# Kernel tuning notes

Measured on AMD Instinct MI355X. Metric: run time of the kernel, lower is better.

The kernel has to match this reference:

```python
import jax, jax.numpy as jnp
import numpy as np

TEMPERATURE = 8.0

def _non_neg(x):
    # exp(x) for x<0, x+1 for x>=0 (non-negative feature map)
    return jnp.where(x < 0, jnp.exp(x), x + 1.0)

def setup_inputs() -> dict:
    key = jax.random.key(0)
    kq, kk, kv, km = jax.random.split(key, 4)
    B, H, S, D = 8, 16, 4096, 64
    q = jax.random.normal(kq, (B, H, S, D), dtype=jnp.float32)
    k = jax.random.normal(kk, (B, H, S, D), dtype=jnp.float32)
    v = jax.random.normal(kv, (B, H, S, D), dtype=jnp.float32)
    token_mask = jax.random.randint(km, (B, S), 0, 2).astype(bool)
    return {"q": q, "k": k, "v": v, "token_mask": token_mask}

def reference(q, k, v, token_mask):
    B, H, S, D = q.shape
    idx = jnp.arange(S, dtype=q.dtype)
    cos_vec = jnp.cos(jnp.pi / 2.0 / S * idx)[:, None]  # [S,1], broadcasts over D
    sin_vec = jnp.sin(jnp.pi / 2.0 / S * idx)[:, None]
    qf = _non_neg(q)
    kf = _non_neg(k)
    q_cos = qf * cos_vec
    q_sin = qf * sin_vec
    k_cos = kf * cos_vec
    k_sin = kf * sin_vec
    mask = token_mask[:, None, :, None].astype(q.dtype)  # [B,1,S,1]
    q_cos = q_cos * mask
    q_sin = q_sin * mask
    # global context: [B,H,D,Dv]
    k_cos_v = jnp.einsum('bhsd,bhse->bhde', k_cos, v)
    k_sin_v = jnp.einsum('bhsd,bhse->bhde', k_sin, v)
    values = (jnp.einsum('bhsd,bhde->bhse', q_cos, k_cos_v)
              + jnp.einsum('bhsd,bhde->bhse', q_sin, k_sin_v)) / TEMPERATURE
    return values
```

## Files before the change

### kernel.cpp

```cpp
#include <hip/hip_runtime.h>
#include <math.h>

#define Sn 4096
#define Dn 64
#define CW 3.834951969714103e-4f
#define P1S 34

typedef __attribute__((ext_vector_type(8))) short short8;
typedef __attribute__((ext_vector_type(4))) float f32x4;

__device__ __forceinline__ unsigned short f2bf(float x) {
    unsigned int u = __float_as_uint(x);
    u += 0x7fffu + ((u >> 16) & 1u);
    return (unsigned short)(u >> 16);
}
__device__ __forceinline__ unsigned int pack2(float lo, float hi) {
    return (unsigned int)f2bf(lo) | ((unsigned int)f2bf(hi) << 16);
}
__device__ __forceinline__ float nneg(float x) {
    return x < 0.f ? __expf(x) : x + 1.f;
}
__device__ __forceinline__ short8 ld_frag(const unsigned int* p) {
    uint2 a = *(const uint2*)p;
    uint2 b = *(const uint2*)(p + 2);
    union { unsigned int u[4]; short8 s; } r;
    r.u[0] = a.x; r.u[1] = a.y; r.u[2] = b.x; r.u[3] = b.y;
    return r.s;
}

__global__ __launch_bounds__(256) void k_init(float4* kv4, int* flag,
                                              const unsigned char* mask_raw) {
    int i = blockIdx.x * 256 + threadIdx.x;
    kv4[i] = make_float4(0.f, 0.f, 0.f, 0.f);
    if (blockIdx.x == 0) {
        __shared__ int s_any;
        if (threadIdx.x == 0) s_any = 0;
        __syncthreads();
        int any = 0;
        int base = threadIdx.x * 16;
        #pragma unroll
        for (int j = 0; j < 16; j++) {
            int idx = base + j;
            if ((idx & 3) && mask_raw[idx]) any = 1;
        }
        if (any) s_any = 1;
        __syncthreads();
        if (threadIdx.x == 0) *flag = s_any ? 0 : 1;
    }
}

__global__ __launch_bounds__(256) void k_phase1(const float* __restrict__ kk,
                                                const float* __restrict__ vv,
                                                float* __restrict__ kv) {
    __shared__ unsigned int ldsKc[64 * P1S];
    __shared__ unsigned int ldsKs[64 * P1S];
    __shared__ unsigned int ldsV [64 * P1S];
    const int t    = threadIdx.x;
    const int bh   = blockIdx.x >> 4;
    const int sblk = (blockIdx.x & 15) << 8;
    const int c    = t & 15;
    const int rp   = t >> 4;
    const int lane = t & 63;
    const int w    = t >> 6;
    const int n    = lane & 15;
    const int q4   = lane >> 4;
    const float* kb = kk + (size_t)bh * (Sn * Dn);
    const float* vb = vv + (size_t)bh * (Sn * Dn);

    f32x4 accC[4], accS[4];
    #pragma unroll
    for (int i = 0; i < 4; i++) {
        accC[i] = (f32x4){0.f, 0.f, 0.f, 0.f};
        accS[i] = (f32x4){0.f, 0.f, 0.f, 0.f};
    }

    float4 pk[2][4], pv[2][4];
    {
        const float* kp = kb + (size_t)(sblk + rp * 4) * Dn + c * 4;
        const float* vp = vb + (size_t)(sblk + rp * 4) * Dn + c * 4;
        #pragma unroll
        for (int i = 0; i < 4; i++) {
            pk[0][i] = *(const float4*)(kp + i * Dn);
            pv[0][i] = *(const float4*)(vp + i * Dn);
        }
    }

    #pragma unroll
    for (int chunk = 0; chunk < 4; chunk++) {
        const int cur = chunk & 1, nxt = cur ^ 1;
        const int s0 = sblk + chunk * 64;
        float cs[4], sn[4], fk[4][4], fv[4][4];
        #pragma unroll
        for (int i = 0; i < 4; i++) {
            __sincosf(CW * (float)(s0 + rp * 4 + i), &sn[i], &cs[i]);
            fk[i][0] = nneg(pk[cur][i].x); fk[i][1] = nneg(pk[cur][i].y);
            fk[i][2] = nneg(pk[cur][i].z); fk[i][3] = nneg(pk[cur][i].w);
            fv[i][0] = pv[cur][i].x; fv[i][1] = pv[cur][i].y;
            fv[i][2] = pv[cur][i].z; fv[i][3] = pv[cur][i].w;
        }
        #pragma unroll
        for (int j = 0; j < 4; j++) {
            int d = c * 4 + j;
            uint2 wc, wsn, wv;
            wc.x  = pack2(fk[0][j] * cs[0], fk[1][j] * cs[1]);
            wc.y  = pack2(fk[2][j] * cs[2], fk[3][j] * cs[3]);
            wsn.x = pack2(fk[0][j] * sn[0], fk[1][j] * sn[1]);
            wsn.y = pack2(fk[2][j] * sn[2], fk[3][j] * sn[3]);
            wv.x  = pack2(fv[0][j], fv[1][j]);
            wv.y  = pack2(fv[2][j], fv[3][j]);
            *(uint2*)&ldsKc[d * P1S + rp * 2] = wc;
            *(uint2*)&ldsKs[d * P1S + rp * 2] = wsn;
            *(uint2*)&ldsV [d * P1S + rp * 2] = wv;
        }
        __syncthreads();
        if (chunk < 3) {
            const float* kp = kb + (size_t)(s0 + 64 + rp * 4) * Dn + c * 4;
            const float* vp = vb + (size_t)(s0 + 64 + rp * 4) * Dn + c * 4;
            #pragma unroll
            for (int i = 0; i < 4; i++) {
                pk[nxt][i] = *(const float4*)(kp + i * Dn);
                pv[nxt][i] = *(const float4*)(vp + i * Dn);
            }
        }
        #pragma unroll
        for (int ks = 0; ks < 2; ks++) {
            short8 Bv = ld_frag(&ldsV[(w * 16 + n) * P1S + ks * 16 + q4 * 4]);
            #pragma unroll
            for (int dt = 0; dt < 4; dt++) {
                short8 Ac = ld_frag(&ldsKc[(dt * 16 + n) * P1S + ks * 16 + q4 * 4]);
                short8 As = ld_frag(&ldsKs[(dt * 16 + n) * P1S + ks * 16 + q4 * 4]);
                accC[dt] = __builtin_amdgcn_mfma_f32_16x16x32_bf16(Ac, Bv, accC[dt], 0, 0, 0);
                accS[dt] = __builtin_amdgcn_mfma_f32_16x16x32_bf16(As, Bv, accS[dt], 0, 0, 0);
            }
        }
        __syncthreads();
    }
    float* base = kv + (size_t)bh * 2 * 4096;
    const int e = w * 16 + n;
    #pragma unroll
    for (int dt = 0; dt < 4; dt++) {
        #pragma unroll
        for (int r = 0; r < 4; r++) {
            int d = dt * 16 + q4 * 4 + r;
            atomicAdd(base +        d * 64 + e, accC[dt][r]);
            atomicAdd(base + 4096 + d * 64 + e, accS[dt][r]);
        }
    }
}

__global__ __launch_bounds__(256) void k_phase2(const float* __restrict__ qq,
                                                const void* __restrict__ mask_raw,
                                                const float* __restrict__ kv,
                                                const int* __restrict__ flag,
                                                float* __restrict__ out) {
    const int t    = threadIdx.x;
    const int bh   = blockIdx.x >> 4;
    const int sblk = (blockIdx.x & 15) << 8;
    const int b    = bh >> 4;
    const int lane = t & 63;
    const int w    = t >> 6;
    const int n    = lane & 15;
    const int q4   = lane >> 4;
    const int iflag = *flag;

    const float* kvb = kv + (size_t)bh * 8192;
    short8 Bc[4][2], Bs[4][2];
    #pragma unroll
    for (int et = 0; et < 4; et++) {
        const int e = et * 16 + n;
        #pragma unroll
        for (int ks = 0; ks < 2; ks++) {
            const int d0 = ks * 32 + q4 * 8;
            union { unsigned int u[4]; short8 s; } uc, us;
            #pragma unroll
            for (int jj = 0; jj < 4; jj++) {
                float c0 = kvb[(size_t)(d0 + 2 * jj)     * 64 + e];
                float c1 = kvb[(size_t)(d0 + 2 * jj + 1) * 64 + e];
                float s0 = kvb[4096 + (size_t)(d0 + 2 * jj)     * 64 + e];
                float s1 = kvb[4096 + (size_t)(d0 + 2 * jj + 1) * 64 + e];
                uc.u[jj] = pack2(c0, c1);
                us.u[jj] = pack2(s0, s1);
            }
            Bc[et][ks] = uc.s;
            Bs[et][ks] = us.s;
        }
    }

    const float* qb = qq + (size_t)bh * (Sn * Dn);
    float* ob       = out + (size_t)bh * (Sn * Dn);
    const unsigned char* m8 = (const unsigned char*)mask_raw;
    const int* m32          = (const int*)mask_raw;

    float4 pq[2][4];
    float  pmv[2];
    {
        int s_row = sblk + w * 16 + n;
        const float* qp = qb + (size_t)s_row * Dn + q4 * 8;
        pq[0][0] = *(const float4*)(qp);
        pq[0][1] = *(const float4*)(qp + 4);
        pq[0][2] = *(const float4*)(qp + 32);
        pq[0][3] = *(const float4*)(qp + 36);
        pmv[0] = iflag ? (m32[b * Sn + s_row] ? 1.f : 0.f)
                       : (m8 [b * Sn + s_row] ? 1.f : 0.f);
    }

    #pragma unroll
    for (int strip = 0; strip < 4; strip++) {
        const int cur = strip & 1, nxt = cur ^ 1;
        const int s_base = sblk + strip * 64 + w * 16;
        const int s_row  = s_base + n;
        float cs, snv;
        __sincosf(CW * (float)s_row, &snv, &cs);
        cs *= pmv[cur]; snv *= pmv[cur];
        float f[16];
        f[0]  = nneg(pq[cur][0].x); f[1]  = nneg(pq[cur][0].y);
        f[2]  = nneg(pq[cur][0].z); f[3]  = nneg(pq[cur][0].w);
        f[4]  = nneg(pq[cur][1].x); f[5]  = nneg(pq[cur][1].y);
        f[6]  = nneg(pq[cur][1].z); f[7]  = nneg(pq[cur][1].w);
        f[8]  = nneg(pq[cur][2].x); f[9]  = nneg(pq[cur][2].y);
        f[10] = nneg(pq[cur][2].z); f[11] = nneg(pq[cur][2].w);
        f[12] = nneg(pq[cur][3].x); f[13] = nneg(pq[cur][3].y);
        f[14] = nneg(pq[cur][3].z); f[15] = nneg(pq[cur][3].w);
        short8 Ac0, As0, Ac1, As1;
        #pragma unroll
        for (int j = 0; j < 8; j++) {
            Ac0[j] = (short)f2bf(f[j] * cs);
            As0[j] = (short)f2bf(f[j] * snv);
            Ac1[j] = (short)f2bf(f[8 + j] * cs);
            As1[j] = (short)f2bf(f[8 + j] * snv);
        }
        if (strip < 3) {
            int s_row2 = sblk + (strip + 1) * 64 + w * 16 + n;
            const float* qp = qb + (size_t)s_row2 * Dn + q4 * 8;
            pq[nxt][0] = *(const float4*)(qp);
            pq[nxt][1] = *(const float4*)(qp + 4);
            pq[nxt][2] = *(const float4*)(qp + 32);
            pq[nxt][3] = *(const float4*)(qp + 36);
            pmv[nxt] = iflag ? (m32[b * Sn + s_row2] ? 1.f : 0.f)
                             : (m8 [b * Sn + s_row2] ? 1.f : 0.f);
        }
        f32x4 acc[4];
        #pragma unroll
        for (int et = 0; et < 4; et++) acc[et] = (f32x4){0.f, 0.f, 0.f, 0.f};
        #pragma unroll
        for (int et = 0; et < 4; et++) {
            acc[et] = __builtin_amdgcn_mfma_f32_16x16x32_bf16(Ac0, Bc[et][0], acc[et], 0, 0, 0);
            acc[et] = __builtin_amdgcn_mfma_f32_16x16x32_bf16(Ac1, Bc[et][1], acc[et], 0, 0, 0);
            acc[et] = __builtin_amdgcn_mfma_f32_16x16x32_bf16(As0, Bs[et][0], acc[et], 0, 0, 0);
            acc[et] = __builtin_amdgcn_mfma_f32_16x16x32_bf16(As1, Bs[et][1], acc[et], 0, 0, 0);
        }
        #pragma unroll
        for (int et = 0; et < 4; et++) {
            #pragma unroll
            for (int r = 0; r < 4; r++) {
                int row = q4 * 4 + r;
                ob[(size_t)(s_base + row) * 64 + et * 16 + n] = acc[et][r] * 0.125f;
            }
        }
    }
}

extern "C" void kernel_launch(void* const* d_in, const int* in_sizes, int n_in,
                              void* d_out, int out_size, void* d_ws, size_t ws_size,
                              hipStream_t stream) {
    const float* q = (const float*)d_in[0];
    const float* k = (const float*)d_in[1];
    const float* v = (const float*)d_in[2];
    const void* mask = d_in[3];
    int*   flag = (int*)d_ws;
    float* kv   = (float*)((char*)d_ws + 256);

    k_init  <<<1024, 256, 0, stream>>>((float4*)kv, flag, (const unsigned char*)mask);
    k_phase1<<<2048, 256, 0, stream>>>(k, v, kv);
    k_phase2<<<2048, 256, 0, stream>>>(q, mask, kv, flag, (float*)d_out);
}
```

Measured before the change: 424.4 us.

## Double-buffer phase1 LDS, halve its grid, and use cheaper bf16 packing

Phase1 now double-buffers its LDS tiles, which removes the trailing barrier in each chunk. Each block also processes 512 sequence rows instead of 256, halving the grid and the number of atomic adds into the global context. The bf16 conversion switches from round-to-nearest-even to a round-half-up add followed by a byte permute, in both phases. Rounding changes slightly, LDS use doubles, and fewer blocks may lower occupancy and parallelism.

```diff
diff --git a/kernel.cpp b/kernel.cpp
--- a/kernel.cpp
+++ b/kernel.cpp
@@ -5,17 +5,15 @@
 #define Dn 64
 #define CW 3.834951969714103e-4f
 #define P1S 34
+#define LDSU (64 * P1S)
 
 typedef __attribute__((ext_vector_type(8))) short short8;
 typedef __attribute__((ext_vector_type(4))) float f32x4;
 
-__device__ __forceinline__ unsigned short f2bf(float x) {
-    unsigned int u = __float_as_uint(x);
-    u += 0x7fffu + ((u >> 16) & 1u);
-    return (unsigned short)(u >> 16);
-}
 __device__ __forceinline__ unsigned int pack2(float lo, float hi) {
-    return (unsigned int)f2bf(lo) | ((unsigned int)f2bf(hi) << 16);
+    unsigned int a = __float_as_uint(lo) + 0x8000u;
+    unsigned int b = __float_as_uint(hi) + 0x8000u;
+    return __builtin_amdgcn_perm(b, a, 0x07060302u);
 }
 __device__ __forceinline__ float nneg(float x) {
     return x < 0.f ? __expf(x) : x + 1.f;
@@ -52,12 +50,10 @@
 __global__ __launch_bounds__(256) void k_phase1(const float* __restrict__ kk,
                                                 const float* __restrict__ vv,
                                                 float* __restrict__ kv) {
-    __shared__ unsigned int ldsKc[64 * P1S];
-    __shared__ unsigned int ldsKs[64 * P1S];
-    __shared__ unsigned int ldsV [64 * P1S];
+    __shared__ unsigned int lds[2 * 3 * LDSU];
     const int t    = threadIdx.x;
-    const int bh   = blockIdx.x >> 4;
-    const int sblk = (blockIdx.x & 15) << 8;
+    const int bh   = blockIdx.x >> 3;
+    const int sblk = (blockIdx.x & 7) << 9;
     const int c    = t & 15;
     const int rp   = t >> 4;
     const int lane = t & 63;
@@ -86,9 +82,12 @@
     }
 
     #pragma unroll
-    for (int chunk = 0; chunk < 4; chunk++) {
+    for (int chunk = 0; chunk < 8; chunk++) {
         const int cur = chunk & 1, nxt = cur ^ 1;
         const int s0 = sblk + chunk * 64;
+        unsigned int* bKc = lds + cur * (3 * LDSU);
+        unsigned int* bKs = bKc + LDSU;
+        unsigned int* bV  = bKs + LDSU;
         float cs[4], sn[4], fk[4][4], fv[4][4];
         #pragma unroll
         for (int i = 0; i < 4; i++) {
@@ -108,12 +107,12 @@
             wsn.y = pack2(fk[2][j] * sn[2], fk[3][j] * sn[3]);
             wv.x  = pack2(fv[0][j], fv[1][j]);
             wv.y  = pack2(fv[2][j], fv[3][j]);
-            *(uint2*)&ldsKc[d * P1S + rp * 2] = wc;
-            *(uint2*)&ldsKs[d * P1S + rp * 2] = wsn;
-            *(uint2*)&ldsV [d * P1S + rp * 2] = wv;
+            *(uint2*)&bKc[d * P1S + rp * 2] = wc;
+            *(uint2*)&bKs[d * P1S + rp * 2] = wsn;
+            *(uint2*)&bV [d * P1S + rp * 2] = wv;
         }
         __syncthreads();
-        if (chunk < 3) {
+        if (chunk < 7) {
             const float* kp = kb + (size_t)(s0 + 64 + rp * 4) * Dn + c * 4;
             const float* vp = vb + (size_t)(s0 + 64 + rp * 4) * Dn + c * 4;
             #pragma unroll
@@ -124,16 +123,15 @@
         }
         #pragma unroll
         for (int ks = 0; ks < 2; ks++) {
-            short8 Bv = ld_frag(&ldsV[(w * 16 + n) * P1S + ks * 16 + q4 * 4]);
+            short8 Bv = ld_frag(&bV[(w * 16 + n) * P1S + ks * 16 + q4 * 4]);
             #pragma unroll
             for (int dt = 0; dt < 4; dt++) {
-                short8 Ac = ld_frag(&ldsKc[(dt * 16 + n) * P1S + ks * 16 + q4 * 4]);
-                short8 As = ld_frag(&ldsKs[(dt * 16 + n) * P1S + ks * 16 + q4 * 4]);
+                short8 Ac = ld_frag(&bKc[(dt * 16 + n) * P1S + ks * 16 + q4 * 4]);
+                short8 As = ld_frag(&bKs[(dt * 16 + n) * P1S + ks * 16 + q4 * 4]);
                 accC[dt] = __builtin_amdgcn_mfma_f32_16x16x32_bf16(Ac, Bv, accC[dt], 0, 0, 0);
                 accS[dt] = __builtin_amdgcn_mfma_f32_16x16x32_bf16(As, Bv, accS[dt], 0, 0, 0);
             }
         }
-        __syncthreads();
     }
     float* base = kv + (size_t)bh * 2 * 4096;
     const int e = w * 16 + n;
@@ -221,13 +219,13 @@
         f[10] = nneg(pq[cur][2].z); f[11] = nneg(pq[cur][2].w);
         f[12] = nneg(pq[cur][3].x); f[13] = nneg(pq[cur][3].y);
         f[14] = nneg(pq[cur][3].z); f[15] = nneg(pq[cur][3].w);
-        short8 Ac0, As0, Ac1, As1;
-        #pragma unroll
-        for (int j = 0; j < 8; j++) {
-            Ac0[j] = (short)f2bf(f[j] * cs);
-            As0[j] = (short)f2bf(f[j] * snv);
-            Ac1[j] = (short)f2bf(f[8 + j] * cs);
-            As1[j] = (short)f2bf(f[8 + j] * snv);
+        union { unsigned int u[4]; short8 s; } ac0, as0, ac1, as1;
+        #pragma unroll
+        for (int j = 0; j < 4; j++) {
+            ac0.u[j] = pack2(f[2*j]     * cs,  f[2*j + 1]     * cs);
+            as0.u[j] = pack2(f[2*j]     * snv, f[2*j + 1]     * snv);
+            ac1.u[j] = pack2(f[8 + 2*j] * cs,  f[8 + 2*j + 1] * cs);
+            as1.u[j] = pack2(f[8 + 2*j] * snv, f[8 + 2*j + 1] * snv);
         }
         if (strip < 3) {
             int s_row2 = sblk + (strip + 1) * 64 + w * 16 + n;
@@ -244,10 +242,10 @@
         for (int et = 0; et < 4; et++) acc[et] = (f32x4){0.f, 0.f, 0.f, 0.f};
         #pragma unroll
         for (int et = 0; et < 4; et++) {
-            acc[et] = __builtin_amdgcn_mfma_f32_16x16x32_bf16(Ac0, Bc[et][0], acc[et], 0, 0, 0);
-            acc[et] = __builtin_amdgcn_mfma_f32_16x16x32_bf16(Ac1, Bc[et][1], acc[et], 0, 0, 0);
-            acc[et] = __builtin_amdgcn_mfma_f32_16x16x32_bf16(As0, Bs[et][0], acc[et], 0, 0, 0);
-            acc[et] = __builtin_amdgcn_mfma_f32_16x16x32_bf16(As1, Bs[et][1], acc[et], 0, 0, 0);
+            acc[et] = __builtin_amdgcn_mfma_f32_16x16x32_bf16(ac0.s, Bc[et][0], acc[et], 0, 0, 0);
+            acc[et] = __builtin_amdgcn_mfma_f32_16x16x32_bf16(ac1.s, Bc[et][1], acc[et], 0, 0, 0);
+            acc[et] = __builtin_amdgcn_mfma_f32_16x16x32_bf16(as0.s, Bs[et][0], acc[et], 0, 0, 0);
+            acc[et] = __builtin_amdgcn_mfma_f32_16x16x32_bf16(as1.s, Bs[et][1], acc[et], 0, 0, 0);
         }
         #pragma unroll
         for (int et = 0; et < 4; et++) {
@@ -271,6 +269,6 @@
     float* kv   = (float*)((char*)d_ws + 256);
 
     k_init  <<<1024, 256, 0, stream>>>((float4*)kv, flag, (const unsigned char*)mask);
-    k_phase1<<<2048, 256, 0, stream>>>(k, v, kv);
+    k_phase1<<<1024, 256, 0, stream>>>(k, v, kv);
     k_phase2<<<2048, 256, 0, stream>>>(q, mask, kv, flag, (float*)d_out);
 }
```

Result: no change. 419.5 us (-1.2%).
